# Kernel tuning notes

Hardware: AMD Instinct MI355X
Metric: run time of the kernel (lower is better)

Reference implementation:

```python
import jax, jax.numpy as jnp
import numpy as np

B, S, D, E = 8, 2048, 4096, 64
EXPERT_CAPACITY = 40  # seq_len / n_experts * 1.25


def setup_inputs() -> dict:
    key = jax.random.key(0)
    k1, k2 = jax.random.split(key)
    hidden_states = jax.random.normal(k1, (B, S, D), dtype=jnp.float32)
    W = jax.random.normal(k2, (D, E), dtype=jnp.float32) * (1.0 / np.sqrt(D))
    b = jnp.zeros((E,), dtype=jnp.float32)
    return {"hidden_states": hidden_states, "W": W, "b": b}


def reference(hidden_states, W, b):
    # router logits: [B, S, E] (jitter_noise == 0, router_dtype == float32)
    router_logits = jnp.einsum('bsd,de->bse', hidden_states, W) + b
    router_probs = jax.nn.softmax(router_logits, axis=-1)
    top1_probs = jnp.max(router_probs, axis=-1)                    # [B, S]
    expert_idx = jnp.argmax(router_probs, axis=-1)                 # [B, S]
    expert_indices = jax.nn.one_hot(expert_idx, E, dtype=jnp.int32)  # [B, S, E]
    # capacity masking: cumulative token priority per expert along seq dim
    token_priority = jnp.cumsum(expert_indices, axis=-2)           # [B, S, E]
    capacity_mask = token_priority <= EXPERT_CAPACITY
    expert_indices = expert_indices * capacity_mask.astype(jnp.int32)
    num_dropped = jnp.sum(jnp.sum(expert_indices, axis=-1) == 0)
    # aux load-balancing loss
    fi = jnp.sum(expert_indices, axis=-2).astype(router_probs.dtype) / S  # [B, E]
    pi = jnp.sum(router_probs, axis=-2) / S                               # [B, E]
    aux_loss = jnp.mean(E * jnp.sum(fi * pi, axis=-1))
    return (expert_indices, top1_probs, router_probs, aux_loss, num_dropped)
```

## Files before the change

kernel.cpp:

```cpp
#include <hip/hip_runtime.h>
#include <hip/hip_bf16.h>
#include <stdint.h>

#define Bb 8
#define Ss 2048
#define Dd 4096
#define Ee 64
#define CAP 40
#define M_TOK (Bb*Ss)
#define TOP1_OFF  (M_TOK*Ee)
#define PROBS_OFF (TOP1_OFF + M_TOK)
#define AUX_OFF   (PROBS_OFF + M_TOK*Ee)
#define ND_OFF    (AUX_OFF + 1)

#define W2_OFF   0u
#define PART_OFF (1u<<20)
#define CNTT_OFF (17u<<20)
#define PIT_OFF  ((17u<<20) + (64u<<10))
#define EID_OFF  ((17u<<20) + (128u<<10))

typedef __attribute__((ext_vector_type(8))) short short8;
typedef __attribute__((ext_vector_type(4))) float f32x4;

#define FENCE() do {                                                          \
    asm volatile("" ::: "memory");                                            \
    __builtin_amdgcn_sched_barrier(0);                                        \
  } while (0)

__device__ __forceinline__ void cvt8hl(const float4 a, const float4 b,
                                       short8& hi, short8& lo) {
  __hip_bfloat162 h0 = __float22bfloat162_rn(make_float2(a.x, a.y));
  __hip_bfloat162 h1 = __float22bfloat162_rn(make_float2(a.z, a.w));
  __hip_bfloat162 h2 = __float22bfloat162_rn(make_float2(b.x, b.y));
  __hip_bfloat162 h3 = __float22bfloat162_rn(make_float2(b.z, b.w));
  float2 f0 = __bfloat1622float2(h0), f1 = __bfloat1622float2(h1);
  float2 f2 = __bfloat1622float2(h2), f3 = __bfloat1622float2(h3);
  __hip_bfloat162 l0 = __float22bfloat162_rn(make_float2(a.x - f0.x, a.y - f0.y));
  __hip_bfloat162 l1 = __float22bfloat162_rn(make_float2(a.z - f1.x, a.w - f1.y));
  __hip_bfloat162 l2 = __float22bfloat162_rn(make_float2(b.x - f2.x, b.y - f2.y));
  __hip_bfloat162 l3 = __float22bfloat162_rn(make_float2(b.z - f3.x, b.w - f3.y));
  union U { __hip_bfloat162 h[4]; short8 s; };
  U uh; uh.h[0] = h0; uh.h[1] = h1; uh.h[2] = h2; uh.h[3] = h3; hi = uh.s;
  U ul; ul.h[0] = l0; ul.h[1] = l1; ul.h[2] = l2; ul.h[3] = l3; lo = ul.s;
}

__global__ __launch_bounds__(256) void k0_wsplit(const float* __restrict__ W,
                                                 char* __restrict__ w2) {
  const int id  = blockIdx.x * 256 + threadIdx.x;
  const int l   = id & 63;
  const int g   = (id >> 6) & 3;
  const int sub = (id >> 8) & 1;
  const int c   = id >> 9;
  const int e   = g * 16 + (l & 15);
  const int kb  = c * 64 + sub * 32 + (l >> 4) * 8;
  float xs[8];
#pragma unroll
  for (int j = 0; j < 8; ++j) xs[j] = W[(size_t)(kb + j) * Ee + e];
  short8 hi, lo;
  cvt8hl(make_float4(xs[0], xs[1], xs[2], xs[3]),
         make_float4(xs[4], xs[5], xs[6], xs[7]), hi, lo);
  char* base = w2 + (size_t)c * 16384 + sub * 8192 + g * 2048 + l * 16;
  *(short8*)base = hi;
  *(short8*)(base + 1024) = lo;
}

__global__ __launch_bounds__(256, 6) void k1_gemm(
    const float* __restrict__ H, const char* __restrict__ w2,
    float* __restrict__ part) {
  __shared__ char wb[2][8192];
  const int tid = threadIdx.x;
  const int wv = tid >> 6, l = tid & 63;
  const int tg = blockIdx.x >> 2, ks = blockIdx.x & 3;
  const float* hA = H + (size_t)(tg * 64 + wv * 16 + (l & 15)) * Dd
                      + ks * 1024 + (l >> 4) * 8;
  const char* wsrc = w2 + (size_t)ks * 262144 + wv * 2048 + l * 16;

  f32x4 acc[4];
#pragma unroll
  for (int g = 0; g < 4; ++g) acc[g] = (f32x4){0.f, 0.f, 0.f, 0.f};

  float4 aX0, aX1, aY0, aY1;
  short8 ah0, al0;

#define GLL16(gs, ls)                                                         \
  __builtin_amdgcn_global_load_lds(                                           \
      (const __attribute__((address_space(1))) unsigned int*)(gs),            \
      (__attribute__((address_space(3))) unsigned int*)(ls), 16, 0, 0)

#define STAGE(t, bi) {                                                        \
    const char* s_ = wsrc + (size_t)(t) * 8192;                               \
    char* d_ = &wb[bi][wv * 2048];                                            \
    GLL16(s_, d_); GLL16(s_ + 1024, d_ + 1024); }

#define LDA(r0, r1, t) { const float* p_ = hA + (t) * 32;                     \
    r0 = *(const float4*)(p_); r1 = *(const float4*)(p_ + 4); }

#define MFMA4(ac, ah, al, wh, wl) {                                           \
    ac = __builtin_amdgcn_mfma_f32_16x16x32_bf16(ah, wh, ac, 0, 0, 0);        \
    ac = __builtin_amdgcn_mfma_f32_16x16x32_bf16(ah, wl, ac, 0, 0, 0);        \
    ac = __builtin_amdgcn_mfma_f32_16x16x32_bf16(al, wh, ac, 0, 0, 0);        \
    ac = __builtin_amdgcn_mfma_f32_16x16x32_bf16(al, wl, ac, 0, 0, 0); }

#define COMPM(bi) { const char* wp_ = &wb[bi][0] + l * 16;                    \
    _Pragma("unroll")                                                         \
    for (int g = 0; g < 4; ++g) {                                             \
      const short8 wh = *(const short8*)(wp_ + g * 2048);                     \
      const short8 wl = *(const short8*)(wp_ + g * 2048 + 1024);              \
      MFMA4(acc[g], ah0, al0, wh, wl);                                        \
    } }

  STAGE(0, 0);
  FENCE();
  LDA(aX0, aX1, 0);
  LDA(aY0, aY1, 1);
  FENCE();
  asm volatile("s_waitcnt vmcnt(4)" ::: "memory");
  __builtin_amdgcn_s_barrier();

#pragma unroll
  for (int t = 0; t < 32; ++t) {
    const int bi = t & 1;
    if (t < 31) STAGE(t + 1, bi ^ 1);
    FENCE();
    if ((t & 1) == 0) {
      cvt8hl(aX0, aX1, ah0, al0);
      if (t < 30) LDA(aX0, aX1, t + 2);
    } else {
      cvt8hl(aY0, aY1, ah0, al0);
      if (t < 30) LDA(aY0, aY1, t + 2);
    }
    FENCE();
    COMPM(bi);
    if (t < 30)       { asm volatile("s_waitcnt vmcnt(2)" ::: "memory"); }
    else if (t == 30) { asm volatile("s_waitcnt vmcnt(0)" ::: "memory"); }
    if (t < 31) __builtin_amdgcn_s_barrier();
  }

  float* pp = part + (size_t)(tg * 4 + ks) * 4096;
#pragma unroll
  for (int g = 0; g < 4; ++g)
#pragma unroll
    for (int r = 0; r < 4; ++r)
      pp[(wv * 16 + (l >> 4) * 4 + r) * 64 + g * 16 + (l & 15)] = acc[g][r];
}

__global__ __launch_bounds__(512) void k1b_softmax(
    const float* __restrict__ part, const float* __restrict__ bias,
    float* __restrict__ out, int* __restrict__ cntT, float* __restrict__ piT,
    int* __restrict__ eid_ws) {
  __shared__ int   csh[512];
  __shared__ float psh[512];
  const int tid = threadIdx.x, wv = tid >> 6, l = tid & 63;
  const int tg = blockIdx.x;
  const float* p0 = part + (size_t)tg * 16384;

  int cnt = 0; float pis = 0.f;
  const float bl_ = bias[l];
#pragma unroll
  for (int i = 0; i < 8; ++i) {
    const int t = wv * 8 + i, tok = tg * 64 + t;
    const float v = p0[t * 64 + l] + p0[4096 + t * 64 + l] +
                    p0[8192 + t * 64 + l] + p0[12288 + t * 64 + l] + bl_;
    float m = v; int mi = l;
#pragma unroll
    for (int off = 32; off >= 1; off >>= 1) {
      const float ov = __shfl_xor(m, off);
      const int   oi = __shfl_xor(mi, off);
      if (ov > m || (ov == m && oi < mi)) { m = ov; mi = oi; }
    }
    const float ex = __expf(v - m);
    float ssum = ex;
#pragma unroll
    for (int off = 32; off >= 1; off >>= 1) ssum += __shfl_xor(ssum, off);
    const float inv = 1.0f / ssum;
    const float p = ex * inv;
    out[(size_t)PROBS_OFF + (size_t)tok * Ee + l] = p;
    if (l == 0) {
      out[TOP1_OFF + tok] = inv;
      eid_ws[tok] = mi;
    }
    cnt += (mi == l) ? 1 : 0;
    pis += p;
  }
  csh[wv * 64 + l] = cnt;
  psh[wv * 64 + l] = pis;
  __syncthreads();
  if (tid < 64) {
    int ct = 0; float pp = 0.f;
#pragma unroll
    for (int w = 0; w < 8; ++w) { ct += csh[w * 64 + tid]; pp += psh[w * 64 + tid]; }
    cntT[((size_t)(tg >> 5) * 64 + tid) * 32 + (tg & 31)] = ct;
    piT [((size_t)(tg >> 5) * 64 + tid) * 32 + (tg & 31)] = pp;
  }
}

__global__ __launch_bounds__(64) void k3_indices(
    const int* __restrict__ cntT, const float* __restrict__ piT,
    const int* __restrict__ eid_ws, float* __restrict__ out) {
  __shared__ float tile[64][64];
  const int g = blockIdx.x, lane = threadIdx.x;
  const int b = g >> 5, cc = g & 31;
  const int tok = g * 64 + lane;
  const int e = eid_ws[tok];

  unsigned long long mymask = 0ull;
  for (int j = 0; j < 64; ++j) {
    const int ej = __shfl(e, j);
    const unsigned long long bal = __ballot(ej == e);
    if (j == lane) mymask = bal;
  }
  const int lrank = __popcll(mymask & ((1ull << lane) - 1ull));

  const int4* cp = (const int4*)(cntT + ((size_t)b * 64 + e) * 32);
  int prefix = 0;
#pragma unroll
  for (int j = 0; j < 8; ++j) {
    const int4 v = cp[j];
    const int base = 4 * j;
    prefix += ((base + 0 < cc) ? v.x : 0) + ((base + 1 < cc) ? v.y : 0)
            + ((base + 2 < cc) ? v.z : 0) + ((base + 3 < cc) ? v.w : 0);
  }
  const float keep = (prefix + lrank < CAP) ? 1.0f : 0.0f;

#pragma unroll
  for (int j = 0; j < 64; ++j) tile[j][lane] = 0.f;
  __syncthreads();
  tile[lane][e] = keep;
  __syncthreads();

  float4*       og = (float4*)(out + (size_t)g * 64 * 64);
  const float4* ts = (const float4*)&tile[0][0];
#pragma unroll
  for (int i = 0; i < 16; ++i) og[i * 64 + lane] = ts[i * 64 + lane];

  if (g == 0) {
    float auxsum = 0.f; int dropped = 0;
    for (int bb = 0; bb < 8; ++bb) {
      const int4*   cq = (const int4*)  (cntT + ((size_t)bb * 64 + lane) * 32);
      const float4* pq = (const float4*)(piT  + ((size_t)bb * 64 + lane) * 32);
      int tot = 0; float ps = 0.f;
#pragma unroll
      for (int j = 0; j < 8; ++j) {
        const int4 v = cq[j];   tot += v.x + v.y + v.z + v.w;
        const float4 w = pq[j]; ps  += w.x + w.y + w.z + w.w;
      }
      dropped += (tot > CAP) ? (tot - CAP) : 0;
      const float fi = (float)((tot < CAP) ? tot : CAP) * (1.0f / (float)Ss);
      const float pi = ps * (1.0f / (float)Ss);
      float fp = fi * pi;
#pragma unroll
      for (int off = 32; off >= 1; off >>= 1) fp += __shfl_xor(fp, off);
      auxsum += fp;
    }
#pragma unroll
    for (int off = 32; off >= 1; off >>= 1) dropped += __shfl_xor(dropped, off);
    if (lane == 0) {
      out[AUX_OFF] = (float)Ee * auxsum / (float)Bb;
      out[ND_OFF]  = (float)dropped;
    }
  }
}

extern "C" void kernel_launch(void* const* d_in, const int* in_sizes, int n_in,
                              void* d_out, int out_size, void* d_ws, size_t ws_size,
                              hipStream_t stream) {
  const float* H    = (const float*)d_in[0];
  const float* Wm   = (const float*)d_in[1];
  const float* bias = (const float*)d_in[2];
  float* out = (float*)d_out;
  char*  w2   = (char*) d_ws + W2_OFF;
  float* part = (float*)((char*)d_ws + PART_OFF);
  int*   cntT = (int*)  ((char*)d_ws + CNTT_OFF);
  float* piT  = (float*)((char*)d_ws + PIT_OFF);
  int*   eid  = (int*)  ((char*)d_ws + EID_OFF);

  hipLaunchKernelGGL(k0_wsplit,   dim3(128),  dim3(256), 0, stream, Wm, w2);
  hipLaunchKernelGGL(k1_gemm,     dim3(1024), dim3(256), 0, stream, H, w2, part);
  hipLaunchKernelGGL(k1b_softmax, dim3(256),  dim3(512), 0, stream,
                     part, bias, out, cntT, piT, eid);
  hipLaunchKernelGGL(k3_indices,  dim3(256),  dim3(64),  0, stream,
                     cntT, piT, eid, out);
}
```

Baseline: 92.11 us.

## Load router weights directly into registers instead of staging through LDS

The GEMM kernel stops staging the pre-split bf16 weight tile through a double-buffered LDS array with global_load_lds and barriers. Each wave now loads all four expert groups' weight fragments straight from global memory into a double-buffered set of registers, and the block barriers are removed. Occupancy launch bounds drop from 6 to 4 to make room for the extra registers. In exchange, each wave fetches the full weight tile itself, so global/L2 weight traffic rises fourfold, and occupancy falls.

```diff
diff --git a/kernel.cpp b/kernel.cpp
--- a/kernel.cpp
+++ b/kernel.cpp
@@ -64,16 +64,15 @@
   *(short8*)(base + 1024) = lo;
 }
 
-__global__ __launch_bounds__(256, 6) void k1_gemm(
+__global__ __launch_bounds__(256, 4) void k1_gemm(
     const float* __restrict__ H, const char* __restrict__ w2,
     float* __restrict__ part) {
-  __shared__ char wb[2][8192];
   const int tid = threadIdx.x;
   const int wv = tid >> 6, l = tid & 63;
   const int tg = blockIdx.x >> 2, ks = blockIdx.x & 3;
   const float* hA = H + (size_t)(tg * 64 + wv * 16 + (l & 15)) * Dd
                       + ks * 1024 + (l >> 4) * 8;
-  const char* wsrc = w2 + (size_t)ks * 262144 + wv * 2048 + l * 16;
+  const char* wsrc = w2 + (size_t)ks * 262144 + l * 16;
 
   f32x4 acc[4];
 #pragma unroll
@@ -81,19 +80,18 @@
 
   float4 aX0, aX1, aY0, aY1;
   short8 ah0, al0;
-
-#define GLL16(gs, ls)                                                         \
-  __builtin_amdgcn_global_load_lds(                                           \
-      (const __attribute__((address_space(1))) unsigned int*)(gs),            \
-      (__attribute__((address_space(3))) unsigned int*)(ls), 16, 0, 0)
-
-#define STAGE(t, bi) {                                                        \
-    const char* s_ = wsrc + (size_t)(t) * 8192;                               \
-    char* d_ = &wb[bi][wv * 2048];                                            \
-    GLL16(s_, d_); GLL16(s_ + 1024, d_ + 1024); }
+  short8 wa0, wa1, wa2, wa3, wa4, wa5, wa6, wa7;
+  short8 wb0, wb1, wb2, wb3, wb4, wb5, wb6, wb7;
 
 #define LDA(r0, r1, t) { const float* p_ = hA + (t) * 32;                     \
     r0 = *(const float4*)(p_); r1 = *(const float4*)(p_ + 4); }
+
+#define LDW(q0, q1, q2, q3, q4, q5, q6, q7, t) {                              \
+    const char* p_ = wsrc + (size_t)(t) * 8192;                               \
+    q0 = *(const short8*)(p_);        q1 = *(const short8*)(p_ + 1024);       \
+    q2 = *(const short8*)(p_ + 2048); q3 = *(const short8*)(p_ + 3072);       \
+    q4 = *(const short8*)(p_ + 4096); q5 = *(const short8*)(p_ + 5120);       \
+    q6 = *(const short8*)(p_ + 6144); q7 = *(const short8*)(p_ + 7168); }
 
 #define MFMA4(ac, ah, al, wh, wl) {                                           \
     ac = __builtin_amdgcn_mfma_f32_16x16x32_bf16(ah, wh, ac, 0, 0, 0);        \
@@ -101,39 +99,34 @@
     ac = __builtin_amdgcn_mfma_f32_16x16x32_bf16(al, wh, ac, 0, 0, 0);        \
     ac = __builtin_amdgcn_mfma_f32_16x16x32_bf16(al, wl, ac, 0, 0, 0); }
 
-#define COMPM(bi) { const char* wp_ = &wb[bi][0] + l * 16;                    \
-    _Pragma("unroll")                                                         \
-    for (int g = 0; g < 4; ++g) {                                             \
-      const short8 wh = *(const short8*)(wp_ + g * 2048);                     \
-      const short8 wl = *(const short8*)(wp_ + g * 2048 + 1024);              \
-      MFMA4(acc[g], ah0, al0, wh, wl);                                        \
-    } }
-
-  STAGE(0, 0);
+#define ITER(aU0, aU1, c0, c1, c2, c3, c4, c5, c6, c7,                        \
+             n0, n1, n2, n3, n4, n5, n6, n7, t) {                             \
+    if ((t) == 31) { asm volatile("s_waitcnt vmcnt(0)" ::: "memory"); }       \
+    else           { asm volatile("s_waitcnt vmcnt(2)" ::: "memory"); }       \
+    FENCE();                                                                  \
+    cvt8hl(aU0, aU1, ah0, al0);                                               \
+    FENCE();                                                                  \
+    if ((t) < 31) LDW(n0, n1, n2, n3, n4, n5, n6, n7, (t) + 1);               \
+    if ((t) < 30) LDA(aU0, aU1, (t) + 2);                                     \
+    FENCE();                                                                  \
+    MFMA4(acc[0], ah0, al0, c0, c1);                                          \
+    MFMA4(acc[1], ah0, al0, c2, c3);                                          \
+    MFMA4(acc[2], ah0, al0, c4, c5);                                          \
+    MFMA4(acc[3], ah0, al0, c6, c7); }
+
+  LDA(aX0, aX1, 0);
   FENCE();
-  LDA(aX0, aX1, 0);
+  LDW(wa0, wa1, wa2, wa3, wa4, wa5, wa6, wa7, 0);
+  FENCE();
   LDA(aY0, aY1, 1);
   FENCE();
-  asm volatile("s_waitcnt vmcnt(4)" ::: "memory");
-  __builtin_amdgcn_s_barrier();
-
-#pragma unroll
-  for (int t = 0; t < 32; ++t) {
-    const int bi = t & 1;
-    if (t < 31) STAGE(t + 1, bi ^ 1);
-    FENCE();
-    if ((t & 1) == 0) {
-      cvt8hl(aX0, aX1, ah0, al0);
-      if (t < 30) LDA(aX0, aX1, t + 2);
-    } else {
-      cvt8hl(aY0, aY1, ah0, al0);
-      if (t < 30) LDA(aY0, aY1, t + 2);
-    }
-    FENCE();
-    COMPM(bi);
-    if (t < 30)       { asm volatile("s_waitcnt vmcnt(2)" ::: "memory"); }
-    else if (t == 30) { asm volatile("s_waitcnt vmcnt(0)" ::: "memory"); }
-    if (t < 31) __builtin_amdgcn_s_barrier();
+
+#pragma unroll
+  for (int cc = 0; cc < 16; ++cc) {
+    ITER(aX0, aX1, wa0, wa1, wa2, wa3, wa4, wa5, wa6, wa7,
+                   wb0, wb1, wb2, wb3, wb4, wb5, wb6, wb7, 2 * cc);
+    ITER(aY0, aY1, wb0, wb1, wb2, wb3, wb4, wb5, wb6, wb7,
+                   wa0, wa1, wa2, wa3, wa4, wa5, wa6, wa7, 2 * cc + 1);
   }
 
   float* pp = part + (size_t)(tg * 4 + ks) * 4096;
```

New measurement: 160.8 us. 74.6% more time.
